# Kernel optimization log

Hardware: AMD Instinct MI355X
Metric: run time of the kernel (lower is better)

Reference implementation:

```python
import jax, jax.numpy as jnp
import numpy as np

N = 8192
IN_CH = 256
OUT_CH = 256


def setup_inputs() -> dict:
    key = jax.random.key(0)
    k1, k2, k3, k4, k5 = jax.random.split(key, 5)
    features = jax.random.normal(k1, (N, IN_CH), dtype=jnp.float32)
    wavelets = jax.random.normal(k2, (N, N), dtype=jnp.float32)
    wavelets_inv = jax.random.normal(k3, (N, N), dtype=jnp.float32)
    # parameters
    # xavier uniform for weight_matrix
    limit = np.sqrt(6.0 / (IN_CH + OUT_CH)).astype(np.float32)
    weight_matrix = jax.random.uniform(k4, (IN_CH, OUT_CH), minval=-limit, maxval=limit, dtype=jnp.float32)
    filt = jax.random.uniform(k5, (N,), minval=0.9, maxval=1.1, dtype=jnp.float32)
    return {"features": features, "wavelets": wavelets, "wavelets_inv": wavelets_inv,
            "weight_matrix": weight_matrix, "filt": filt}


def reference(features, wavelets, wavelets_inv, weight_matrix, filt):
    # transformed = features @ W                    [N, out]
    transformed = features @ weight_matrix
    # spectral = wavelets_inv @ transformed         [N, out]
    spectral = wavelets_inv @ transformed
    # torch.diag(filter) @ spectral == filt[:, None] * spectral (avoid NxN diag GEMM)
    filtered = filt[:, None] * spectral
    # output = wavelets @ filtered                  [N, out]
    return wavelets @ filtered
```

## Files before the change

kernel.cpp:

```cpp
#include <hip/hip_runtime.h>
#include <hip/hip_bf16.h>
#include <stdint.h>
#include <stddef.h>

typedef __bf16 bf16;
typedef float f32x4 __attribute__((ext_vector_type(4)));
typedef bf16 bf16x8 __attribute__((ext_vector_type(8)));
typedef bf16 bf16x4 __attribute__((ext_vector_type(4)));

#define MROWS 8192
#define NOUT 256
#define BK 128
#define NTHREADS 512
#define LDS_SMALL (32 * BK * 2)

#define SCHED0 __builtin_amdgcn_sched_barrier(0)
#define SBAR __builtin_amdgcn_s_barrier()


__global__ __launch_bounds__(NTHREADS, 1) void gemm_ks(
    const float* __restrict__ A, const bf16* __restrict__ Bp,
    float* __restrict__ wsP, float* __restrict__ doutP,
    const int kshift, const int nsteps, const int lda) {
  __shared__ char lds[2][32768];
  const int t = threadIdx.x;
  const int w = t >> 6;
  const int l = t & 63;
  const int ks = blockIdx.x & ((1 << kshift) - 1);
  const int mt = blockIdx.x >> kshift;
  const int m0 = mt * 128;
  const int ts0 = ks * nsteps;
  float* __restrict__ Ps =
      (ks == ((1 << kshift) - 1)) ? doutP : wsP + (size_t)ks * 2097152;

  const float* gAq[8];
#pragma unroll
  for (int q = 0; q < 8; ++q)
    gAq[q] = A + (size_t)(m0 + w * 16 + q * 2 + (l >> 5)) * (size_t)lda +
             (size_t)ts0 * BK + (l & 31) * 4;

  int awoff[8];
#pragma unroll
  for (int q = 0; q < 8; ++q) {
    const int r = w * 16 + q * 2 + (l >> 5);
    awoff[q] = r * 256 + ((((l & 31) * 8)) ^ ((r & 7) << 4));
  }

  int aoffb[4];
#pragma unroll
  for (int ak = 0; ak < 4; ++ak)
    aoffb[ak] = (l & 15) * 256 +
                ((ak * 64 + (l >> 4) * 16) ^ ((l & 7) << 4));

  const char* pBw = (const char*)Bp + w * 8192 + l * 16;

  f32x4 acc[8][2] = {};
  f32x4 pA[8];
  bf16x8 Ba[2][4], Bb[2][4];

#pragma unroll
  for (int q = 0; q < 8; ++q) pA[q] = *(const f32x4*)gAq[q];
  SCHED0;
#pragma unroll
  for (int bfi = 0; bfi < 2; ++bfi)
#pragma unroll
    for (int ak = 0; ak < 4; ++ak)
      Ba[bfi][ak] = *(const bf16x8*)(pBw + ((size_t)ts0 << 16) +
                                     (bfi * 4 + ak) * 1024);
  SCHED0;
#pragma unroll
  for (int q = 0; q < 8; ++q) {
    bf16x4 pk;
#pragma unroll
    for (int e = 0; e < 4; ++e) pk[e] = (bf16)pA[q][e];
    *(bf16x4*)(lds[0] + awoff[q]) = pk;
  }
  SCHED0;
  {
    const int s1 = (nsteps > 1) ? BK : 0;
#pragma unroll
    for (int q = 0; q < 8; ++q) pA[q] = *(const f32x4*)(gAq[q] + s1);
  }
  asm volatile("s_waitcnt lgkmcnt(0)" ::: "memory");
  SBAR;
  SCHED0;

#define BODY_K(S, PAR, BCUR, BNXT)                                            \
  {                                                                           \
    const char* rslot = lds[PAR];                                             \
    char* wslot = lds[PAR ^ 1];                                               \
    _Pragma("unroll") for (int q = 0; q < 8; ++q) {                           \
      bf16x4 pk;                                                              \
      _Pragma("unroll") for (int e = 0; e < 4; ++e) pk[e] = (bf16)pA[q][e];   \
      *(bf16x4*)(wslot + awoff[q]) = pk;                                      \
    }                                                                         \
    SCHED0;                                                                   \
    {                                                                         \
      const int tn = ((S) + 1 < nsteps) ? ts0 + (S) + 1 : ts0;                \
      _Pragma("unroll") for (int bfi = 0; bfi < 2; ++bfi)                     \
          _Pragma("unroll") for (int ak = 0; ak < 4; ++ak)                    \
              BNXT[bfi][ak] = *(const bf16x8*)(                               \
                  pBw + ((size_t)tn << 16) + (bfi * 4 + ak) * 1024);          \
    }                                                                         \
    SCHED0;                                                                   \
    {                                                                         \
      const int ka = ((S) + 2 < nsteps) ? ((S) + 2) * BK : 0;                 \
      _Pragma("unroll") for (int q = 0; q < 8; ++q)                           \
          pA[q] = *(const f32x4*)(gAq[q] + ka);                               \
    }                                                                         \
    SCHED0;                                                                   \
    __builtin_amdgcn_s_setprio(1);                                            \
    _Pragma("unroll") for (int ak = 0; ak < 4; ++ak) {                        \
      bf16x8 afr[8];                                                          \
      _Pragma("unroll") for (int af = 0; af < 8; ++af)                        \
          afr[af] = *(const bf16x8*)(rslot + af * 4096 + aoffb[ak]);          \
      _Pragma("unroll") for (int af = 0; af < 8; ++af)                        \
          _Pragma("unroll") for (int bfi = 0; bfi < 2; ++bfi)                 \
              acc[af][bfi] = __builtin_amdgcn_mfma_f32_16x16x32_bf16(         \
                  afr[af], BCUR[bfi][ak], acc[af][bfi], 0, 0, 0);             \
    }                                                                         \
    __builtin_amdgcn_s_setprio(0);                                            \
    SCHED0;                                                                   \
    asm volatile("s_waitcnt lgkmcnt(0)" ::: "memory");                        \
    SBAR;                                                                     \
    SCHED0;                                                                   \
  }

  for (int s = 0; s < nsteps; s += 2) {
    BODY_K(s, 0, Ba, Bb);
    BODY_K(s + 1, 1, Bb, Ba);
  }
#undef BODY_K

#pragma unroll
  for (int af = 0; af < 8; ++af)
#pragma unroll
    for (int bfi = 0; bfi < 2; ++bfi) {
      const int mb = m0 + af * 16 + (l >> 4) * 4;
      const int n = w * 32 + bfi * 16 + (l & 15);
#pragma unroll
      for (int j = 0; j < 4; ++j)
        Ps[(size_t)(mb + j) * NOUT + n] = acc[af][bfi][j];
    }
}

__global__ void reduce2(const float* __restrict__ wsP,
                        const float* __restrict__ doutP,
                        const float* __restrict__ filt, bf16* __restrict__ Fp,
                        const int KS) {
  const int n = threadIdx.x;
  const int m8 = blockIdx.x;
  bf16x8 pk;
#pragma unroll
  for (int r = 0; r < 8; ++r) {
    const int m = m8 * 8 + r;
    float s = doutP[(size_t)m * NOUT + n];
    for (int ks = 0; ks < KS - 1; ++ks)
      s += wsP[(size_t)ks * 2097152 + (size_t)m * NOUT + n];
    pk[r] = (bf16)(s * filt[m]);
  }
  const int ts = m8 >> 4, wq = n >> 5, bq = (n >> 4) & 1, aq = (m8 >> 2) & 3;
  const int lq = (m8 & 3) * 16 + (n & 15);
  *(bf16x8*)((char*)Fp +
             (size_t)(((ts * 64 + wq * 8 + bq * 4 + aq) << 10) + lq * 16)) = pk;
}

__global__ void reduce3(const float* __restrict__ wsP, float* __restrict__ doutP,
                        const int KS) {
  const size_t i = (size_t)blockIdx.x * 256 + threadIdx.x;
  float s = doutP[i];
  for (int ks = 0; ks < KS - 1; ++ks) s += wsP[(size_t)ks * 2097152 + i];
  doutP[i] = s;
}

template <bool SCALE, bool OUTT>
__global__ __launch_bounds__(NTHREADS, 1) void gemm_small(
    const float* __restrict__ A, const bf16* __restrict__ Bp,
    const float* __restrict__ filt, void* __restrict__ outp,
    const int K, const int lda) {
  __shared__ char lds[2][LDS_SMALL];
  const int t = threadIdx.x;
  const int w = t >> 6;
  const int l = t & 63;
  const int m0 = blockIdx.x * 32;
  const int NT = K / BK;

  const int ar = t >> 4;
  const int acb = t & 15;
  const float* gA = A + (size_t)(m0 + ar) * (size_t)lda + acb * 8;
  const int a_lds_off = (ar * (BK * 2) + acb * 16) ^ ((ar & 7) << 4);

  int aoff[2][4];
#pragma unroll
  for (int af = 0; af < 2; ++af)
#pragma unroll
    for (int ak = 0; ak < 4; ++ak) {
      const int r = af * 16 + (l & 15);
      const int kb = ak * 64 + (l >> 4) * 16;
      aoff[af][ak] = (r * (BK * 2) + kb) ^ ((r & 7) << 4);
    }

  const char* pBw = (const char*)Bp + w * 8192 + l * 16;

  f32x4 acc[2][2] = {};

  f32x4 aS0a = __builtin_nontemporal_load((const f32x4*)gA);
  f32x4 aS0b = __builtin_nontemporal_load((const f32x4*)gA + 1);
  f32x4 aS1a = __builtin_nontemporal_load((const f32x4*)(gA + BK));
  f32x4 aS1b = __builtin_nontemporal_load((const f32x4*)(gA + BK) + 1);
  bf16x8 Bc[2][4], Bn[2][4];
#pragma unroll
  for (int bfi = 0; bfi < 2; ++bfi)
#pragma unroll
    for (int ak = 0; ak < 4; ++ak)
      Bc[bfi][ak] = *(const bf16x8*)(pBw + (bfi * 4 + ak) * 1024);
  {
    bf16x8 pk;
#pragma unroll
    for (int j = 0; j < 4; ++j) { pk[j] = (bf16)aS0a[j]; pk[j + 4] = (bf16)aS0b[j]; }
    *(bf16x8*)(lds[0] + a_lds_off) = pk;
  }
  asm volatile("s_waitcnt lgkmcnt(0)" ::: "memory");
  SBAR;
  SCHED0;

#define BODY_S(TS, P, BCUR, BNXT, AW0, AW1, AL0, AL1)                         \
  {                                                                           \
    const char* bb = lds[P];                                                  \
    bf16x8 afr[2][4];                                                         \
    _Pragma("unroll") for (int af = 0; af < 2; ++af)                          \
        _Pragma("unroll") for (int ak = 0; ak < 4; ++ak)                      \
            afr[af][ak] = *(const bf16x8*)(bb + aoff[af][ak]);                \
    SCHED0;                                                                   \
    const size_t kb1 = (size_t)((((TS) + 1) < NT ? ((TS) + 1) : 0)) << 16;    \
    _Pragma("unroll") for (int bfi = 0; bfi < 2; ++bfi)                       \
        _Pragma("unroll") for (int ak = 0; ak < 4; ++ak)                      \
            BNXT[bfi][ak] =                                                   \
                *(const bf16x8*)(pBw + kb1 + (bfi * 4 + ak) * 1024);          \
    SCHED0;                                                                   \
    const int ka2 = (((TS) + 2) < NT ? ((TS) + 2) : 0) * BK;                  \
    AL0 = __builtin_nontemporal_load((const f32x4*)(gA + ka2));               \
    AL1 = __builtin_nontemporal_load((const f32x4*)(gA + ka2) + 1);           \
    SCHED0;                                                                   \
    asm volatile("s_waitcnt lgkmcnt(0)" ::: "memory");                        \
    SCHED0;                                                                   \
    __builtin_amdgcn_s_setprio(1);                                            \
    _Pragma("unroll") for (int ak = 0; ak < 4; ++ak)                          \
        _Pragma("unroll") for (int af = 0; af < 2; ++af)                      \
            _Pragma("unroll") for (int bfi = 0; bfi < 2; ++bfi)               \
                acc[af][bfi] = __builtin_amdgcn_mfma_f32_16x16x32_bf16(       \
                    afr[af][ak], BCUR[bfi][ak], acc[af][bfi], 0, 0, 0);       \
    __builtin_amdgcn_s_setprio(0);                                            \
    SCHED0;                                                                   \
    {                                                                         \
      bf16x8 pk;                                                              \
      _Pragma("unroll") for (int j = 0; j < 4; ++j) {                         \
        pk[j] = (bf16)AW0[j];                                                 \
        pk[j + 4] = (bf16)AW1[j];                                             \
      }                                                                       \
      *(bf16x8*)(lds[P ^ 1] + a_lds_off) = pk;                                \
    }                                                                         \
    asm volatile("s_waitcnt lgkmcnt(0)" ::: "memory");                        \
    SBAR;                                                                     \
    SCHED0;                                                                   \
  }

  for (int ts = 0; ts < NT; ts += 2) {
    BODY_S(ts, 0, Bc, Bn, aS1a, aS1b, aS0a, aS0b);
    BODY_S(ts + 1, 1, Bn, Bc, aS0a, aS0b, aS1a, aS1b);
  }
#undef BODY_S

#pragma unroll
  for (int af = 0; af < 2; ++af)
#pragma unroll
    for (int bfi = 0; bfi < 2; ++bfi) {
      const int mb = m0 + af * 16 + (l >> 4) * 4;
      const int n = w * 32 + bfi * 16 + (l & 15);
      f32x4 v = acc[af][bfi];
      if (SCALE) {
#pragma unroll
        for (int j = 0; j < 4; ++j) v[j] *= filt[mb + j];
      }
      if (OUTT) {
        bf16x4 pv;
#pragma unroll
        for (int j = 0; j < 4; ++j) pv[j] = (bf16)v[j];
        const int tsq = mb >> 7, wq = n >> 5, bq = (n >> 4) & 1, aq = (mb >> 5) & 3;
        const int lq = ((mb >> 3) & 3) * 16 + (n & 15);
        char* dst = (char*)outp +
                    (size_t)(((tsq * 64 + wq * 8 + bq * 4 + aq) << 10) + lq * 16 +
                             (mb & 7) * 2);
        *(bf16x4*)dst = pv;
      } else {
        float* po = (float*)outp + (size_t)mb * NOUT + n;
#pragma unroll
        for (int j = 0; j < 4; ++j) po[(size_t)j * NOUT] = v[j];
      }
    }
}

__global__ void prep_wt(const float* __restrict__ W, bf16* __restrict__ Wp) {
  const int k = blockIdx.x;
  const int n = threadIdx.x;
  const int off = (((k >> 7) * 64 + (n >> 5) * 8 + ((n >> 4) & 1) * 4 +
                    ((k >> 5) & 3)) << 10) +
                  (((k >> 3) & 3) * 16 + (n & 15)) * 16 + (k & 7) * 2;
  *(bf16*)((char*)Wp + off) = (bf16)W[k * 256 + n];
}

extern "C" void kernel_launch(void* const* d_in, const int* in_sizes, int n_in,
                              void* d_out, int out_size, void* d_ws, size_t ws_size,
                              hipStream_t stream) {
  const float* features = (const float*)d_in[0];
  const float* wavelets = (const float*)d_in[1];
  const float* wavelets_inv = (const float*)d_in[2];
  const float* W = (const float*)d_in[3];
  const float* filt = (const float*)d_in[4];
  float* out = (float*)d_out;

  char* ws = (char*)d_ws;
  bf16* Wp = (bf16*)ws;
  bf16* Tp = (bf16*)(ws + 131072);
  bf16* Fp = (bf16*)(ws + 131072 + 4194304);
  float* wsP = (float*)(ws + 131072 + 8388608);

  const size_t base = 131072 + 8388608;
  int KS = 0, kshift = 0;
  if (ws_size >= base + 3u * 8388608u) { KS = 4; kshift = 2; }
  else if (ws_size >= base + 1u * 8388608u) { KS = 2; kshift = 1; }

  prep_wt<<<256, 256, 0, stream>>>(W, Wp);
  gemm_small<false, true><<<256, NTHREADS, 0, stream>>>(features, Wp, nullptr, Tp, 256, 256);

  if (KS) {
    const int nsteps = 64 / KS;
    gemm_ks<<<64 * KS, NTHREADS, 0, stream>>>(wavelets_inv, Tp, wsP, out, kshift, nsteps, 8192);
    reduce2<<<1024, 256, 0, stream>>>(wsP, out, filt, Fp, KS);
    gemm_ks<<<64 * KS, NTHREADS, 0, stream>>>(wavelets, Fp, wsP, out, kshift, nsteps, 8192);
    reduce3<<<8192, 256, 0, stream>>>(wsP, out, KS);
  } else {
    gemm_ks<<<64, NTHREADS, 0, stream>>>(wavelets_inv, Tp, wsP, out, 0, 64, 8192);
    reduce2<<<1024, 256, 0, stream>>>(wsP, out, filt, Fp, 1);
    gemm_ks<<<64, NTHREADS, 0, stream>>>(wavelets, Fp, wsP, out, 0, 64, 8192);
  }
}
```

Measured before the change: 160.6 us.

## Stream fp32 A tiles directly to LDS via global_load_lds, convert at fragment read

The A operand was loaded from global into registers, converted to bf16, and written to LDS by each thread. It is now copied as fp32 straight into a doubled LDS buffer with the direct global-to-LDS load, using an XOR swizzle on source columns. Conversion to bf16 moves to the fragment read, which now issues two LDS reads per fragment plus conversions. This frees registers and removes the LDS store path, but doubles LDS footprint and read traffic and moves conversion into the MFMA loop.

Result: slower. 182.9 us (+13.9%).

```diff
diff --git a/kernel.cpp b/kernel.cpp
--- a/kernel.cpp
+++ b/kernel.cpp
@@ -17,12 +17,18 @@
 #define SCHED0 __builtin_amdgcn_sched_barrier(0)
 #define SBAR __builtin_amdgcn_s_barrier()
 
+__device__ __forceinline__ void glds16(const void* g, const void* l) {
+  __builtin_amdgcn_global_load_lds(
+      (const __attribute__((address_space(1))) void*)g,
+      (__attribute__((address_space(3))) void*)l, 16, 0, 0);
+}
+
 
 __global__ __launch_bounds__(NTHREADS, 1) void gemm_ks(
     const float* __restrict__ A, const bf16* __restrict__ Bp,
     float* __restrict__ wsP, float* __restrict__ doutP,
     const int kshift, const int nsteps, const int lda) {
-  __shared__ char lds[2][32768];
+  __shared__ char lds[2][65536];
   const int t = threadIdx.x;
   const int w = t >> 6;
   const int l = t & 63;
@@ -33,33 +39,31 @@
   float* __restrict__ Ps =
       (ks == ((1 << kshift) - 1)) ? doutP : wsP + (size_t)ks * 2097152;
 
-  const float* gAq[8];
-#pragma unroll
-  for (int q = 0; q < 8; ++q)
-    gAq[q] = A + (size_t)(m0 + w * 16 + q * 2 + (l >> 5)) * (size_t)lda +
-             (size_t)ts0 * BK + (l & 31) * 4;
-
-  int awoff[8];
+  const float* gAsrc[8];
+  int ldst[8];
 #pragma unroll
   for (int q = 0; q < 8; ++q) {
-    const int r = w * 16 + q * 2 + (l >> 5);
-    awoff[q] = r * 256 + ((((l & 31) * 8)) ^ ((r & 7) << 4));
-  }
-
-  int aoffb[4];
+    const int rL = w * 16 + 2 * q + (l >> 5);
+    const int cS = (l & 31) ^ (rL & 7);
+    gAsrc[q] = A + (size_t)(m0 + rL) * (size_t)lda + (size_t)ts0 * BK + cS * 4;
+    ldst[q] = (w * 16 + 2 * q) * 512;
+  }
+
+  int aoffq[4][2];
 #pragma unroll
   for (int ak = 0; ak < 4; ++ak)
-    aoffb[ak] = (l & 15) * 256 +
-                ((ak * 64 + (l >> 4) * 16) ^ ((l & 7) << 4));
+#pragma unroll
+    for (int qq = 0; qq < 2; ++qq)
+      aoffq[ak][qq] = (l & 15) * 512 +
+                      (((ak * 8 + (l >> 4) * 2 + qq) ^ (l & 7)) << 4);
 
   const char* pBw = (const char*)Bp + w * 8192 + l * 16;
 
   f32x4 acc[8][2] = {};
-  f32x4 pA[8];
   bf16x8 Ba[2][4], Bb[2][4];
 
 #pragma unroll
-  for (int q = 0; q < 8; ++q) pA[q] = *(const f32x4*)gAq[q];
+  for (int q = 0; q < 8; ++q) glds16(gAsrc[q], lds[0] + ldst[q]);
   SCHED0;
 #pragma unroll
   for (int bfi = 0; bfi < 2; ++bfi)
@@ -68,31 +72,17 @@
       Ba[bfi][ak] = *(const bf16x8*)(pBw + ((size_t)ts0 << 16) +
                                      (bfi * 4 + ak) * 1024);
   SCHED0;
-#pragma unroll
-  for (int q = 0; q < 8; ++q) {
-    bf16x4 pk;
-#pragma unroll
-    for (int e = 0; e < 4; ++e) pk[e] = (bf16)pA[q][e];
-    *(bf16x4*)(lds[0] + awoff[q]) = pk;
-  }
-  SCHED0;
-  {
-    const int s1 = (nsteps > 1) ? BK : 0;
-#pragma unroll
-    for (int q = 0; q < 8; ++q) pA[q] = *(const f32x4*)(gAq[q] + s1);
-  }
-  asm volatile("s_waitcnt lgkmcnt(0)" ::: "memory");
+  asm volatile("s_waitcnt vmcnt(8)" ::: "memory");
   SBAR;
   SCHED0;
 
 #define BODY_K(S, PAR, BCUR, BNXT)                                            \
   {                                                                           \
     const char* rslot = lds[PAR];                                             \
-    char* wslot = lds[PAR ^ 1];                                               \
-    _Pragma("unroll") for (int q = 0; q < 8; ++q) {                           \
-      bf16x4 pk;                                                              \
-      _Pragma("unroll") for (int e = 0; e < 4; ++e) pk[e] = (bf16)pA[q][e];   \
-      *(bf16x4*)(wslot + awoff[q]) = pk;                                      \
+    {                                                                         \
+      const int ka = ((S) + 1 < nsteps) ? ((S) + 1) * BK : 0;                 \
+      _Pragma("unroll") for (int q = 0; q < 8; ++q)                           \
+          glds16(gAsrc[q] + ka, lds[PAR ^ 1] + ldst[q]);                      \
     }                                                                         \
     SCHED0;                                                                   \
     {                                                                         \
@@ -103,17 +93,19 @@
                   pBw + ((size_t)tn << 16) + (bfi * 4 + ak) * 1024);          \
     }                                                                         \
     SCHED0;                                                                   \
-    {                                                                         \
-      const int ka = ((S) + 2 < nsteps) ? ((S) + 2) * BK : 0;                 \
-      _Pragma("unroll") for (int q = 0; q < 8; ++q)                           \
-          pA[q] = *(const f32x4*)(gAq[q] + ka);                               \
-    }                                                                         \
-    SCHED0;                                                                   \
     __builtin_amdgcn_s_setprio(1);                                            \
     _Pragma("unroll") for (int ak = 0; ak < 4; ++ak) {                        \
       bf16x8 afr[8];                                                          \
-      _Pragma("unroll") for (int af = 0; af < 8; ++af)                        \
-          afr[af] = *(const bf16x8*)(rslot + af * 4096 + aoffb[ak]);          \
+      _Pragma("unroll") for (int af = 0; af < 8; ++af) {                      \
+        f32x4 lo = *(const f32x4*)(rslot + af * 8192 + aoffq[ak][0]);         \
+        f32x4 hi = *(const f32x4*)(rslot + af * 8192 + aoffq[ak][1]);         \
+        bf16x8 v;                                                             \
+        _Pragma("unroll") for (int e = 0; e < 4; ++e) {                       \
+          v[e] = (bf16)lo[e];                                                 \
+          v[e + 4] = (bf16)hi[e];                                             \
+        }                                                                     \
+        afr[af] = v;                                                          \
+      }                                                                       \
       _Pragma("unroll") for (int af = 0; af < 8; ++af)                        \
           _Pragma("unroll") for (int bfi = 0; bfi < 2; ++bfi)                 \
               acc[af][bfi] = __builtin_amdgcn_mfma_f32_16x16x32_bf16(         \
@@ -121,7 +113,7 @@
     }                                                                         \
     __builtin_amdgcn_s_setprio(0);                                            \
     SCHED0;                                                                   \
-    asm volatile("s_waitcnt lgkmcnt(0)" ::: "memory");                        \
+    asm volatile("s_waitcnt vmcnt(8)" ::: "memory");                          \
     SBAR;                                                                     \
     SCHED0;                                                                   \
   }
```
